# Kernel optimization log

Hardware: AMD Instinct MI355X
Metric: run time of the kernel (lower is better)

Reference implementation:

```python
import jax, jax.numpy as jnp
import numpy as np
from jax import lax
from jax.scipy.stats import norm

K = 2            # top-k
NUM_EXPERTS = 4
NOISE_EPS = 0.01
LOSS_COEF = 0.01


def conv3x3(x, w):
    # x: [B,Cin,H,W], w: [Cout,Cin,3,3] -> [B,Cout,H,W]
    return lax.conv_general_dilated(x, w, (1, 1), 'SAME',
                                    dimension_numbers=('NCHW', 'OIHW', 'NCHW'))


def setup_inputs() -> dict:
    key = jax.random.key(0)
    ks = jax.random.split(key, 16)
    B, C, H, W = 16, 3, 256, 256
    FC = 2 * C                      # freq channels = 6
    HID = 64
    D = H * W * C                   # flattened gating dim = 196608
    f32 = jnp.float32
    inp = {
        'x':   jax.random.normal(ks[0], (B, C, H, W), f32),
        'ref': jax.random.normal(ks[1], (B, C, H, W), f32),
        'noise': jax.random.normal(ks[2], (B, NUM_EXPERTS), f32),
        'mod_w1': (jax.random.normal(ks[3], (FC, 2 * FC), f32) * 0.1),
        'mod_b1': jnp.zeros((FC,), f32),
        'mod_w2': (jax.random.normal(ks[4], (FC, FC), f32) * 0.1),
        'mod_b2': jnp.zeros((FC,), f32),
        'enh_w': (jax.random.normal(ks[5], (FC, FC), f32) * 0.1),
        'enh_b': jnp.zeros((FC,), f32),
        'fre_prompt': (jax.random.normal(ks[6], (FC, H, W // 2 + 1), f32) * 0.1),
        'w_gate':  (jax.random.normal(ks[7], (D, NUM_EXPERTS), f32) * 0.002),
        'w_noise': (jax.random.normal(ks[8], (D, NUM_EXPERTS), f32) * 0.002),
        'ew1': (jax.random.normal(ks[9],  (NUM_EXPERTS, HID, C, 3, 3), f32) * 0.05),
        'eb1': jnp.zeros((NUM_EXPERTS, HID), f32),
        'ew2': (jax.random.normal(ks[10], (NUM_EXPERTS, 1, HID, 3, 3), f32) * 0.05),
        'eb2': jnp.zeros((NUM_EXPERTS, 1), f32),
    }
    return inp


def _cv_squared(v):
    # torch .var() is unbiased (ddof=1)
    return jnp.var(v, ddof=1) / (jnp.mean(v) ** 2 + 1e-10)


def _forward(x, ref, noise, mod_w1, mod_b1, mod_w2, mod_b2, enh_w, enh_b,
             fre_prompt, w_gate, w_noise, ew1, eb1, ew2, eb2):
    B, C, H, W = x.shape

    # ---- frequency_prompt(ref) ----
    fft = jnp.fft.rfft2(ref, norm='ortho')                    # [B,C,H,W//2+1]
    freq = jnp.concatenate([fft.real, fft.imag], axis=1)      # [B,2C,H,Wf]
    # Adaptive avg/max pool to (H, W//2+1) are identities at native size
    pooled = jnp.concatenate([freq, freq], axis=1)            # [B,4C,H,Wf]
    m = jnp.einsum('oi,bihw->bohw', mod_w1, pooled) + mod_b1[:, None, None]
    m = jax.nn.relu(m)
    m = jnp.einsum('oi,bihw->bohw', mod_w2, m) + mod_b2[:, None, None]
    enh = m * fre_prompt[None]                                # [B,2C,H,Wf]
    enh = jax.nn.relu(jnp.einsum('oi,bihw->bohw', enh_w, enh) + enh_b[:, None, None])
    re, im = jnp.split(enh, 2, axis=1)
    spatial = jnp.fft.irfft2(re + 1j * im, s=(H, W), norm='ortho')  # [B,C,H,W]
    prompt = jax.nn.softmax(spatial.mean(axis=(2, 3), keepdims=True), axis=1)  # [B,C,1,1]

    # ---- noisy top-k gating ----
    x_ds = (x * prompt + x).reshape(B, -1)                    # [B, H*W*C]
    clean_logits = x_ds @ w_gate                              # [B,E]
    noise_stddev = jax.nn.softplus(x_ds @ w_noise) + NOISE_EPS
    noisy_logits = clean_logits + noise * noise_stddev
    top_vals, top_idx = lax.top_k(noisy_logits, K + 1)        # sorted desc, [B,K+1]
    tk_gates = jax.nn.softmax(top_vals[:, :K], axis=1)        # [B,K]
    gates = jnp.zeros_like(noisy_logits).at[
        jnp.arange(B)[:, None], top_idx[:, :K]].set(tk_gates)  # [B,E]

    # load = prob each expert's noisy logit lands in top-k
    thr_in = top_vals[:, K:K + 1]
    thr_out = top_vals[:, K - 1:K]
    is_in = noisy_logits > thr_in
    prob = jnp.where(is_in,
                     norm.cdf((clean_logits - thr_in) / noise_stddev),
                     norm.cdf((clean_logits - thr_out) / noise_stddev))
    load = prob.sum(0)
    importance = gates.sum(0)
    loss = (_cv_squared(importance) + _cv_squared(load)) * LOSS_COEF

    # ---- expert dispatch/combine (== weighted sum; gates are 0 off top-k) ----
    y = jnp.zeros((B, ew2.shape[1], H, W), x.dtype)
    for e in range(NUM_EXPERTS):
        h = jax.nn.relu(conv3x3(x, ew1[e]) + eb1[e][None, :, None, None])
        o = conv3x3(h, ew2[e]) + eb2[e][None, :, None, None]
        y = y + gates[:, e][:, None, None, None] * o
    return y, loss


def reference(x, ref, noise, mod_w1, mod_b1, mod_w2, mod_b2, enh_w, enh_b,
              fre_prompt, w_gate, w_noise, ew1, eb1, ew2, eb2):
    return _forward(x, ref, noise, mod_w1, mod_b1, mod_w2, mod_b2, enh_w, enh_b,
                    fre_prompt, w_gate, w_noise, ew1, eb1, ew2, eb2)
```

## Files before the change

kernel.cpp:

```cpp
#include <hip/hip_runtime.h>
#include <hip/hip_bf16.h>
#include <math.h>

#define WS_GATE 192
#define WS_GNP  256
#define WS_W1F  25088
#define WS_W2F  29184

typedef float    float4v __attribute__((ext_vector_type(4)));
typedef short    short8v __attribute__((ext_vector_type(8)));
typedef _Float16 half8v  __attribute__((ext_vector_type(8)));

union Q4 { uint4 q; short8v s; half8v h; };

__device__ __forceinline__ unsigned short bf16b(float f) {
    unsigned u = __builtin_bit_cast(unsigned, f);
    u = (u + 0x7FFFu + ((u >> 16) & 1u)) >> 16;
    return (unsigned short)u;
}

__device__ __forceinline__ unsigned pkbf16(float a, float b) {
#if __has_builtin(__builtin_amdgcn_cvt_pk_bf16_f32)
    return __builtin_bit_cast(unsigned, __builtin_amdgcn_cvt_pk_bf16_f32(a, b));
#else
    return (unsigned)bf16b(a) | ((unsigned)bf16b(b) << 16);
#endif
}

__device__ __forceinline__ unsigned pkf16(float a, float b) {
#if __has_builtin(__builtin_amdgcn_cvt_pkrtz)
    return __builtin_bit_cast(unsigned, __builtin_amdgcn_cvt_pkrtz(a, b));
#else
    union { _Float16 h[2]; unsigned u; } p;
    p.h[0] = (_Float16)a; p.h[1] = (_Float16)b;
    return p.u;
#endif
}

__global__ void k_prep(const float* __restrict__ ew1, const float* __restrict__ ew2,
                       float* __restrict__ ws) {
    int t = threadIdx.x;
    uint4* w1f = (uint4*)(ws + WS_W1F);
    for (int i = t; i < 1024; i += 256) {
        int mm = i & 15, r = i >> 4, qq = r & 3, r2 = r >> 2, f = r2 & 3, e = r2 >> 2;
        const float* w1 = ew1 + e*1728 + (f*16 + mm)*27 + qq*8;
        int navail = 27 - qq*8;
        float v[8];
        #pragma unroll
        for (int j = 0; j < 8; ++j) v[j] = (j < navail) ? w1[j] : 0.f;
        uint4 q;
        q.x = pkbf16(v[0], v[1]); q.y = pkbf16(v[2], v[3]);
        q.z = pkbf16(v[4], v[5]); q.w = pkbf16(v[6], v[7]);
        w1f[i] = q;
    }
    uint4* w2f = (uint4*)(ws + WS_W2F);
    for (int i = t; i < 512; i += 256) {
        int qq = i & 3, r = i >> 2, ks = r & 1, r2 = r >> 1, mm = r2 & 15, e = r2 >> 4;
        uint4 q = make_uint4(0, 0, 0, 0);
        if (mm < 9) {
            float v[8];
            #pragma unroll
            for (int j = 0; j < 8; ++j) v[j] = ew2[e*576 + (ks*32 + qq*8 + j)*9 + mm];
            q.x = pkf16(v[0], v[1]); q.y = pkf16(v[2], v[3]);
            q.z = pkf16(v[4], v[5]); q.w = pkf16(v[6], v[7]);
        }
        w2f[i] = q;
    }
}

__global__ void k_refsum(const float* __restrict__ ref, float* __restrict__ ws) {
    int bc = blockIdx.x, chunk = blockIdx.y, t = threadIdx.x;
    const float4* p4 = (const float4*)(ref + (size_t)bc*65536 + (size_t)chunk*16384);
    float acc = 0.f;
    #pragma unroll
    for (int i = 0; i < 16; ++i) { float4 v = p4[i*256 + t]; acc += v.x + v.y + v.z + v.w; }
    #pragma unroll
    for (int m = 1; m <= 32; m <<= 1) acc += __shfl_xor(acc, m);
    __shared__ float red[4];
    if ((t & 63) == 0) red[t >> 6] = acc;
    __syncthreads();
    if (t == 0) ws[bc*4 + chunk] = red[0] + red[1] + red[2] + red[3];
}

__global__ void k_gatedots(const float* __restrict__ x, const float* __restrict__ wg,
                           const float* __restrict__ wn, float* __restrict__ ws) {
    int c = blockIdx.x;
    int chunk = blockIdx.y;
    int t = threadIdx.x, lane = t & 63, wv = t >> 6;
    int hw0 = chunk*1024 + t*4;
    const float4* wg4 = (const float4*)wg;
    const float4* wn4 = (const float4*)wn;
    const float4* x4  = (const float4*)x;
    float4 G[4], Nw[4];
    #pragma unroll
    for (int i = 0; i < 4; ++i) {
        G[i]  = wg4[c*65536 + hw0 + i];
        Nw[i] = wn4[c*65536 + hw0 + i];
    }
    __shared__ float part[4][16][8];
    for (int b = 0; b < 16; ++b) {
        float4 xv = x4[(b*3 + c)*16384 + chunk*256 + t];
        float xs[4] = {xv.x, xv.y, xv.z, xv.w};
        float aG[4] = {0,0,0,0}, aN[4] = {0,0,0,0};
        #pragma unroll
        for (int i = 0; i < 4; ++i) {
            aG[0] += xs[i]*G[i].x;  aG[1] += xs[i]*G[i].y;
            aG[2] += xs[i]*G[i].z;  aG[3] += xs[i]*G[i].w;
            aN[0] += xs[i]*Nw[i].x; aN[1] += xs[i]*Nw[i].y;
            aN[2] += xs[i]*Nw[i].z; aN[3] += xs[i]*Nw[i].w;
        }
        #pragma unroll
        for (int m = 1; m <= 32; m <<= 1) {
            #pragma unroll
            for (int e = 0; e < 4; ++e) {
                aG[e] += __shfl_xor(aG[e], m);
                aN[e] += __shfl_xor(aN[e], m);
            }
        }
        if (lane == 0) {
            #pragma unroll
            for (int e = 0; e < 4; ++e) { part[wv][b][e] = aG[e]; part[wv][b][4+e] = aN[e]; }
        }
    }
    __syncthreads();
    if (t < 128) {
        int b = t >> 3, s = t & 7;
        float v = part[0][b][s] + part[1][b][s] + part[2][b][s] + part[3][b][s];
        ws[WS_GNP + ((size_t)(c*64 + chunk)*16 + b)*8 + s] = v;
    }
}

__global__ void k_gating(const float* __restrict__ noise,
                         const float* __restrict__ mw1, const float* __restrict__ mb1,
                         const float* __restrict__ mw2, const float* __restrict__ mb2,
                         const float* __restrict__ enw, const float* __restrict__ enb,
                         const float* __restrict__ fp,
                         float* __restrict__ ws, float* __restrict__ out) {
    __shared__ float GN2[48*8];
    __shared__ float gL[16][4], pL[16][4], cvs[2];
    int t = threadIdx.x;
    #pragma unroll
    for (int u = 0; u < 3; ++u) {
        int idx = t*3 + u;
        int bc = idx >> 3, s = idx & 7;
        int b = bc / 3, c = bc - b*3;
        float v = 0.f;
        for (int ch = 0; ch < 64; ++ch)
            v += ws[WS_GNP + ((size_t)(c*64 + ch)*16 + b)*8 + s];
        GN2[bc*8 + s] = v;
    }
    __syncthreads();
    if (t < 16) {
        int b = t;
        float sc[3];
        for (int c = 0; c < 3; ++c) {
            int bc = b*3 + c;
            sc[c] = (ws[bc*4] + ws[bc*4+1] + ws[bc*4+2] + ws[bc*4+3]) * (1.f/256.f);
        }
        float pooled[12];
        for (int i = 0; i < 12; ++i) { int r = i % 6; pooled[i] = (r < 3) ? sc[r] : 0.f; }
        float m1[6];
        for (int o = 0; o < 6; ++o) {
            float a = mb1[o];
            for (int i = 0; i < 12; ++i) a += mw1[o*12 + i] * pooled[i];
            m1[o] = fmaxf(a, 0.f);
        }
        float m2[6];
        for (int o = 0; o < 6; ++o) {
            float a = mb2[o];
            for (int i = 0; i < 6; ++i) a += mw2[o*6 + i] * m1[i];
            m2[o] = a * fp[(size_t)o * 33024];
        }
        float dc[3];
        for (int o = 0; o < 3; ++o) {
            float a = enb[o];
            for (int i = 0; i < 6; ++i) a += enw[o*6 + i] * m2[i];
            dc[o] = fmaxf(a, 0.f) * (1.f/256.f);
        }
        float mx = fmaxf(dc[0], fmaxf(dc[1], dc[2]));
        float e0 = expf(dc[0]-mx), e1 = expf(dc[1]-mx), e2 = expf(dc[2]-mx);
        float inv = 1.f / (e0 + e1 + e2);
        float pc[3] = { e0*inv + 1.f, e1*inv + 1.f, e2*inv + 1.f };
        float cl[4], sg[4], nz[4];
        for (int e = 0; e < 4; ++e) {
            float a = 0.f, nr = 0.f;
            for (int c = 0; c < 3; ++c) {
                a  += pc[c] * GN2[(b*3 + c)*8 + e];
                nr += pc[c] * GN2[(b*3 + c)*8 + 4 + e];
            }
            cl[e] = a;
            float sp = (nr > 20.f) ? nr : log1pf(expf(nr));
            sg[e] = sp + 0.01f;
            nz[e] = a + noise[b*4 + e] * sg[e];
        }
        int i0 = 0; float v0 = nz[0];
        for (int e = 1; e < 4; ++e) if (nz[e] > v0) { v0 = nz[e]; i0 = e; }
        int i1 = -1; float v1 = -3.4e38f;
        for (int e = 0; e < 4; ++e) if (e != i0 && nz[e] > v1) { v1 = nz[e]; i1 = e; }
        float v2 = -3.4e38f;
        for (int e = 0; e < 4; ++e) if (e != i0 && e != i1 && nz[e] > v2) v2 = nz[e];
        float ex = expf(v1 - v0), den = 1.f + ex;
        float gate[4] = {0.f, 0.f, 0.f, 0.f};
        gate[i0] = 1.f/den; gate[i1] = ex/den;
        for (int e = 0; e < 4; ++e) {
            ws[WS_GATE + b*4 + e] = gate[e];
            gL[b][e] = gate[e];
            float thr = (nz[e] > v2) ? v2 : v1;
            pL[b][e] = 0.5f * (1.f + erff((cl[e] - thr) / sg[e] * 0.70710678118f));
        }
    }
    __syncthreads();
    if (t < 2) {
        float v[4];
        for (int e = 0; e < 4; ++e) {
            float s = 0.f;
            for (int b = 0; b < 16; ++b) s += (t == 0) ? gL[b][e] : pL[b][e];
            v[e] = s;
        }
        float mean = 0.25f * (v[0] + v[1] + v[2] + v[3]);
        float var = 0.f;
        for (int e = 0; e < 4; ++e) { float d = v[e] - mean; var += d*d; }
        var *= (1.f/3.f);
        cvs[t] = var / (mean*mean + 1e-10f);
    }
    __syncthreads();
    if (t == 0) out[1048576] = (cvs[0] + cvs[1]) * 0.01f;
}

__global__ __launch_bounds__(256, 3)
void k_experts(const float* __restrict__ x,  const float* __restrict__ eb1,
               const float* __restrict__ eb2, const float* __restrict__ ws,
               float* __restrict__ out) {
    __shared__ __align__(16) uint4 s_hid[324*8];
    __shared__ __align__(16) char  s_mix[5904];
    float*    in_s = (float*)s_mix;
    _Float16* s_T  = (_Float16*)s_mix;

    int t = threadIdx.x;
    int b = blockIdx.x >> 8, tile = blockIdx.x & 255;
    int ty0 = (tile >> 4) * 16, tx0 = (tile & 15) * 16;
    const float* xb = x + (size_t)b * 196608;

    for (int i = t; i < 1200; i += 256) {
        int ci = i / 400, r = i - ci*400, iy = r / 20, ix = r - iy*20;
        int gy = ty0 - 2 + iy, gx = tx0 - 2 + ix;
        float v = 0.f;
        if ((unsigned)gy < 256u && (unsigned)gx < 256u) v = xb[ci*65536 + gy*256 + gx];
        in_s[i] = v;
    }
    __syncthreads();

    int lane = t & 63, wv = t >> 6;
    int qq = lane >> 4, mm = lane & 15;
    int oy = t >> 4, ox = t & 15;

    int offj[8];
    #pragma unroll
    for (int j = 0; j < 8; ++j) {
        int k = qq*8 + j;
        if (k < 27) { int ci = k/9, r = k - ci*9, kh = r/3, kw = r - kh*3;
                      offj[j] = ci*400 + kh*20 + kw; }
        else offj[j] = -1;
    }

    Q4 bfr[6];
    #pragma unroll
    for (int i = 0; i < 6; ++i) {
        int gidx = wv + i*4;
        if (gidx >= 21) break;
        int p = gidx*16 + mm;
        int py = p/18, px = p - py*18;
        int base = (p < 324) ? (py*20 + px) : 0;
        float v[8];
        #pragma unroll
        for (int j = 0; j < 8; ++j)
            v[j] = (offj[j] >= 0) ? in_s[base + offj[j]] : 0.f;
        bfr[i].q.x = pkbf16(v[0], v[1]); bfr[i].q.y = pkbf16(v[2], v[3]);
        bfr[i].q.z = pkbf16(v[4], v[5]); bfr[i].q.w = pkbf16(v[6], v[7]);
    }

    bool interior = (ty0 > 0) && (ty0 < 240) && (tx0 > 0) && (tx0 < 240);
    const float4 gates = *(const float4*)(ws + WS_GATE + b*4);
    float gv[4] = {gates.x, gates.y, gates.z, gates.w};
    const uint4* w1f = (const uint4*)(ws + WS_W1F);
    const uint4* w2f = (const uint4*)(ws + WS_W2F);
    float accY = 0.f;

    for (int e = 0; e < 4; ++e) {
        float g = gv[e];
        if (g == 0.f) continue;

        Q4 bw0, bw1;
        bw0.q = w2f[((e*16 + mm)*2 + 0)*4 + qq];
        bw1.q = w2f[((e*16 + mm)*2 + 1)*4 + qq];

        Q4 af[4];
        float4 bias[4];
        #pragma unroll
        for (int f = 0; f < 4; ++f) {
            af[f].q = w1f[((e*4 + f)*4 + qq)*16 + mm];
            bias[f] = *(const float4*)(eb1 + e*64 + f*16 + qq*4);
        }

        #pragma unroll
        for (int i = 0; i < 6; ++i) {
            int gidx = wv + i*4;
            if (gidx >= 21) break;
            int p = gidx*16 + mm;
            bool valid = p < 324;
            float msk = 1.f;
            if (!interior) {
                int py = p/18, px = p - py*18;
                int gy = ty0 - 1 + py, gx = tx0 - 1 + px;
                msk = (((unsigned)gy < 256u) && ((unsigned)gx < 256u)) ? 1.f : 0.f;
            }
            #pragma unroll
            for (int f = 0; f < 4; ++f) {
                float4v d = __builtin_amdgcn_mfma_f32_16x16x32_bf16(
                    af[f].s, bfr[i].s, (float4v){0.f,0.f,0.f,0.f}, 0, 0, 0);
                if (valid) {
                    float h0 = fmaxf(d[0] + bias[f].x, 0.f);
                    float h1 = fmaxf(d[1] + bias[f].y, 0.f);
                    float h2 = fmaxf(d[2] + bias[f].z, 0.f);
                    float h3 = fmaxf(d[3] + bias[f].w, 0.f);
                    if (!interior) { h0 *= msk; h1 *= msk; h2 *= msk; h3 *= msk; }
                    uint2 pk = make_uint2(pkf16(h0, h1), pkf16(h2, h3));
                    int ch0 = f*16 + qq*4;
                    int hchunk = ch0 >> 3, hsel = (ch0 >> 2) & 1;
                    ((uint2*)&s_hid[p*8 + ((hchunk + p) & 7)])[hsel] = pk;
                }
            }
        }
        __syncthreads();

        for (int gi = wv; gi < 21; gi += 4) {
            int base = gi*16; if (base > 308) base = 308;
            int p = base + mm;
            Q4 a0, a1;
            a0.q = s_hid[p*8 + ((qq + p) & 7)];
            a1.q = s_hid[p*8 + ((4 + qq + p) & 7)];
            float4v d = __builtin_amdgcn_mfma_f32_16x16x32_f16(
                a0.h, bw0.h, (float4v){0.f,0.f,0.f,0.f}, 0, 0, 0);
            d = __builtin_amdgcn_mfma_f32_16x16x32_f16(a1.h, bw1.h, d, 0, 0, 0);
            if (mm < 9) {
                *(uint2*)&s_T[mm*328 + base + qq*4] =
                    make_uint2(pkf16(d[0], d[1]), pkf16(d[2], d[3]));
            }
        }
        __syncthreads();

        float oacc = 0.f;
        #pragma unroll
        for (int kh = 0; kh < 3; ++kh) {
            #pragma unroll
            for (int kw = 0; kw < 3; ++kw)
                oacc += (float)s_T[(kh*3 + kw)*328 + (oy + kh)*18 + ox + kw];
        }
        accY += g * (oacc + eb2[e]);
    }
    out[(size_t)b*65536 + (ty0 + oy)*256 + tx0 + ox] = accY;
}

extern "C" void kernel_launch(void* const* d_in, const int* in_sizes, int n_in,
                              void* d_out, int out_size, void* d_ws, size_t ws_size,
                              hipStream_t stream) {
    (void)in_sizes; (void)n_in; (void)out_size; (void)ws_size;
    const float* x     = (const float*)d_in[0];
    const float* ref   = (const float*)d_in[1];
    const float* noise = (const float*)d_in[2];
    const float* mw1   = (const float*)d_in[3];
    const float* mb1   = (const float*)d_in[4];
    const float* mw2   = (const float*)d_in[5];
    const float* mb2   = (const float*)d_in[6];
    const float* enw   = (const float*)d_in[7];
    const float* enb   = (const float*)d_in[8];
    const float* fp    = (const float*)d_in[9];
    const float* wg    = (const float*)d_in[10];
    const float* wn    = (const float*)d_in[11];
    const float* ew1   = (const float*)d_in[12];
    const float* eb1   = (const float*)d_in[13];
    const float* ew2   = (const float*)d_in[14];
    const float* eb2   = (const float*)d_in[15];
    float* out = (float*)d_out;
    float* ws  = (float*)d_ws;

    k_prep    <<<1, 256, 0, stream>>>(ew1, ew2, ws);
    k_refsum  <<<dim3(48, 4),  256, 0, stream>>>(ref, ws);
    k_gatedots<<<dim3(3, 64),  256, 0, stream>>>(x, wg, wn, ws);
    k_gating  <<<1, 128, 0, stream>>>(noise, mw1, mb1, mw2, mb2, enw, enb, fp, ws, out);
    k_experts <<<4096, 256, 0, stream>>>(x, eb1, eb2, ws, out);
}
```

Before: 195.9 us.

## Merge prep, refsum and gate-dot kernels into one launch; fold bias into MFMA

Merges the three independent preprocessing kernels (weight packing, ref sums, gating dot products) into a single k_aux launch that dispatches on block index, cutting two kernel launches and their serialization gaps. It also feeds the first-layer bias as the MFMA accumulator init instead of adding it after the matrix op, which removes four adds per tile. The trade-off is a larger combined kernel whose resource use is set by the heaviest branch.

```diff
diff --git a/kernel.cpp b/kernel.cpp
--- a/kernel.cpp
+++ b/kernel.cpp
@@ -37,9 +37,72 @@
 #endif
 }
 
-__global__ void k_prep(const float* __restrict__ ew1, const float* __restrict__ ew2,
-                       float* __restrict__ ws) {
-    int t = threadIdx.x;
+__global__ void k_aux(const float* __restrict__ ref, const float* __restrict__ x,
+                      const float* __restrict__ wg,  const float* __restrict__ wn,
+                      const float* __restrict__ ew1, const float* __restrict__ ew2,
+                      float* __restrict__ ws) {
+    __shared__ float sh[4][16][8];
+    int blk = blockIdx.x, t = threadIdx.x;
+
+    if (blk < 192) {
+        int bc = blk >> 2, chunk = blk & 3;
+        const float4* p4 = (const float4*)(ref + (size_t)bc*65536 + (size_t)chunk*16384);
+        float acc = 0.f;
+        #pragma unroll
+        for (int i = 0; i < 16; ++i) { float4 v = p4[i*256 + t]; acc += v.x + v.y + v.z + v.w; }
+        #pragma unroll
+        for (int m = 1; m <= 32; m <<= 1) acc += __shfl_xor(acc, m);
+        if ((t & 63) == 0) sh[0][0][t >> 6] = acc;
+        __syncthreads();
+        if (t == 0) ws[bc*4 + chunk] = sh[0][0][0] + sh[0][0][1] + sh[0][0][2] + sh[0][0][3];
+        return;
+    }
+    if (blk < 384) {
+        int r = blk - 192;
+        int c = r >> 6, chunk = r & 63;
+        int lane = t & 63, wv = t >> 6;
+        int hw0 = chunk*1024 + t*4;
+        const float4* wg4 = (const float4*)wg;
+        const float4* wn4 = (const float4*)wn;
+        const float4* x4  = (const float4*)x;
+        float4 G[4], Nw[4];
+        #pragma unroll
+        for (int i = 0; i < 4; ++i) {
+            G[i]  = wg4[c*65536 + hw0 + i];
+            Nw[i] = wn4[c*65536 + hw0 + i];
+        }
+        for (int b = 0; b < 16; ++b) {
+            float4 xv = x4[(b*3 + c)*16384 + chunk*256 + t];
+            float xs[4] = {xv.x, xv.y, xv.z, xv.w};
+            float aG[4] = {0,0,0,0}, aN[4] = {0,0,0,0};
+            #pragma unroll
+            for (int i = 0; i < 4; ++i) {
+                aG[0] += xs[i]*G[i].x;  aG[1] += xs[i]*G[i].y;
+                aG[2] += xs[i]*G[i].z;  aG[3] += xs[i]*G[i].w;
+                aN[0] += xs[i]*Nw[i].x; aN[1] += xs[i]*Nw[i].y;
+                aN[2] += xs[i]*Nw[i].z; aN[3] += xs[i]*Nw[i].w;
+            }
+            #pragma unroll
+            for (int m = 1; m <= 32; m <<= 1) {
+                #pragma unroll
+                for (int e = 0; e < 4; ++e) {
+                    aG[e] += __shfl_xor(aG[e], m);
+                    aN[e] += __shfl_xor(aN[e], m);
+                }
+            }
+            if (lane == 0) {
+                #pragma unroll
+                for (int e = 0; e < 4; ++e) { sh[wv][b][e] = aG[e]; sh[wv][b][4+e] = aN[e]; }
+            }
+        }
+        __syncthreads();
+        if (t < 128) {
+            int b = t >> 3, s = t & 7;
+            float v = sh[0][b][s] + sh[1][b][s] + sh[2][b][s] + sh[3][b][s];
+            ws[WS_GNP + ((size_t)(c*64 + chunk)*16 + b)*8 + s] = v;
+        }
+        return;
+    }
     uint4* w1f = (uint4*)(ws + WS_W1F);
     for (int i = t; i < 1024; i += 256) {
         int mm = i & 15, r = i >> 4, qq = r & 3, r2 = r >> 2, f = r2 & 3, e = r2 >> 2;
@@ -65,68 +128,6 @@
             q.z = pkf16(v[4], v[5]); q.w = pkf16(v[6], v[7]);
         }
         w2f[i] = q;
-    }
-}
-
-__global__ void k_refsum(const float* __restrict__ ref, float* __restrict__ ws) {
-    int bc = blockIdx.x, chunk = blockIdx.y, t = threadIdx.x;
-    const float4* p4 = (const float4*)(ref + (size_t)bc*65536 + (size_t)chunk*16384);
-    float acc = 0.f;
-    #pragma unroll
-    for (int i = 0; i < 16; ++i) { float4 v = p4[i*256 + t]; acc += v.x + v.y + v.z + v.w; }
-    #pragma unroll
-    for (int m = 1; m <= 32; m <<= 1) acc += __shfl_xor(acc, m);
-    __shared__ float red[4];
-    if ((t & 63) == 0) red[t >> 6] = acc;
-    __syncthreads();
-    if (t == 0) ws[bc*4 + chunk] = red[0] + red[1] + red[2] + red[3];
-}
-
-__global__ void k_gatedots(const float* __restrict__ x, const float* __restrict__ wg,
-                           const float* __restrict__ wn, float* __restrict__ ws) {
-    int c = blockIdx.x;
-    int chunk = blockIdx.y;
-    int t = threadIdx.x, lane = t & 63, wv = t >> 6;
-    int hw0 = chunk*1024 + t*4;
-    const float4* wg4 = (const float4*)wg;
-    const float4* wn4 = (const float4*)wn;
-    const float4* x4  = (const float4*)x;
-    float4 G[4], Nw[4];
-    #pragma unroll
-    for (int i = 0; i < 4; ++i) {
-        G[i]  = wg4[c*65536 + hw0 + i];
-        Nw[i] = wn4[c*65536 + hw0 + i];
-    }
-    __shared__ float part[4][16][8];
-    for (int b = 0; b < 16; ++b) {
-        float4 xv = x4[(b*3 + c)*16384 + chunk*256 + t];
-        float xs[4] = {xv.x, xv.y, xv.z, xv.w};
-        float aG[4] = {0,0,0,0}, aN[4] = {0,0,0,0};
-        #pragma unroll
-        for (int i = 0; i < 4; ++i) {
-            aG[0] += xs[i]*G[i].x;  aG[1] += xs[i]*G[i].y;
-            aG[2] += xs[i]*G[i].z;  aG[3] += xs[i]*G[i].w;
-            aN[0] += xs[i]*Nw[i].x; aN[1] += xs[i]*Nw[i].y;
-            aN[2] += xs[i]*Nw[i].z; aN[3] += xs[i]*Nw[i].w;
-        }
-        #pragma unroll
-        for (int m = 1; m <= 32; m <<= 1) {
-            #pragma unroll
-            for (int e = 0; e < 4; ++e) {
-                aG[e] += __shfl_xor(aG[e], m);
-                aN[e] += __shfl_xor(aN[e], m);
-            }
-        }
-        if (lane == 0) {
-            #pragma unroll
-            for (int e = 0; e < 4; ++e) { part[wv][b][e] = aG[e]; part[wv][b][4+e] = aN[e]; }
-        }
-    }
-    __syncthreads();
-    if (t < 128) {
-        int b = t >> 3, s = t & 7;
-        float v = part[0][b][s] + part[1][b][s] + part[2][b][s] + part[3][b][s];
-        ws[WS_GNP + ((size_t)(c*64 + chunk)*16 + b)*8 + s] = v;
     }
 }
 
@@ -295,11 +296,12 @@
         bw1.q = w2f[((e*16 + mm)*2 + 1)*4 + qq];
 
         Q4 af[4];
-        float4 bias[4];
+        float4v cinit[4];
         #pragma unroll
         for (int f = 0; f < 4; ++f) {
             af[f].q = w1f[((e*4 + f)*4 + qq)*16 + mm];
-            bias[f] = *(const float4*)(eb1 + e*64 + f*16 + qq*4);
+            float4 bb = *(const float4*)(eb1 + e*64 + f*16 + qq*4);
+            cinit[f] = (float4v){bb.x, bb.y, bb.z, bb.w};
         }
 
         #pragma unroll
@@ -317,12 +319,12 @@
             #pragma unroll
             for (int f = 0; f < 4; ++f) {
                 float4v d = __builtin_amdgcn_mfma_f32_16x16x32_bf16(
-                    af[f].s, bfr[i].s, (float4v){0.f,0.f,0.f,0.f}, 0, 0, 0);
+                    af[f].s, bfr[i].s, cinit[f], 0, 0, 0);
                 if (valid) {
-                    float h0 = fmaxf(d[0] + bias[f].x, 0.f);
-                    float h1 = fmaxf(d[1] + bias[f].y, 0.f);
-                    float h2 = fmaxf(d[2] + bias[f].z, 0.f);
-                    float h3 = fmaxf(d[3] + bias[f].w, 0.f);
+                    float h0 = fmaxf(d[0], 0.f);
+                    float h1 = fmaxf(d[1], 0.f);
+                    float h2 = fmaxf(d[2], 0.f);
+                    float h3 = fmaxf(d[3], 0.f);
                     if (!interior) { h0 *= msk; h1 *= msk; h2 *= msk; h3 *= msk; }
                     uint2 pk = make_uint2(pkf16(h0, h1), pkf16(h2, h3));
                     int ch0 = f*16 + qq*4;
@@ -384,9 +386,7 @@
     float* out = (float*)d_out;
     float* ws  = (float*)d_ws;
 
-    k_prep    <<<1, 256, 0, stream>>>(ew1, ew2, ws);
-    k_refsum  <<<dim3(48, 4),  256, 0, stream>>>(ref, ws);
-    k_gatedots<<<dim3(3, 64),  256, 0, stream>>>(x, wg, wn, ws);
-    k_gating  <<<1, 128, 0, stream>>>(noise, mw1, mb1, mw2, mb2, enw, enb, fp, ws, out);
-    k_experts <<<4096, 256, 0, stream>>>(x, eb1, eb2, ws, out);
-}
+    k_aux    <<<385, 256, 0, stream>>>(ref, x, wg, wn, ew1, ew2, ws);
+    k_gating <<<1, 128, 0, stream>>>(noise, mw1, mb1, mw2, mb2, enw, enb, fp, ws, out);
+    k_experts<<<4096, 256, 0, stream>>>(x, eb1, eb2, ws, out);
+}
```

New measurement: 187.7 us. 1.04x faster.
